# Kernel optimization log

Hardware: AMD Instinct MI355X
Metric: run time of the kernel (lower is better)

The kernel has to match this reference:

```python
import jax, jax.numpy as jnp
import numpy as np

IMG_W, IMG_H = 704, 256
BN_EPS, LN_EPS = 1e-5, 1e-5


def _l2norm(x, axis):
    n = jnp.linalg.norm(x, axis=axis, keepdims=True)
    return x / jnp.maximum(n, 1e-12)


def _layernorm(x, g, b):
    m = jnp.mean(x, axis=-1, keepdims=True)
    v = jnp.var(x, axis=-1, keepdims=True)
    return (x - m) / jnp.sqrt(v + LN_EPS) * g + b


def _bilinear(ref, uv):
    # ref: (B, d, H, W); uv: (B, P, 2) pixel coords (x, y)
    B, d, H, W = ref.shape
    x, y = uv[..., 0], uv[..., 1]
    x0 = jnp.floor(x); y0 = jnp.floor(y)
    wx = x - x0; wy = y - y0
    valid = (x >= 0) & (x <= W - 1) & (y >= 0) & (y <= H - 1)
    x0i = jnp.clip(x0.astype(jnp.int32), 0, W - 1)
    x1i = jnp.clip(x0i + 1, 0, W - 1)
    y0i = jnp.clip(y0.astype(jnp.int32), 0, H - 1)
    y1i = jnp.clip(y0i + 1, 0, H - 1)
    ref_t = ref.reshape(B, d, H * W).transpose(0, 2, 1)  # (B, HW, d)
    g = lambda yy, xx: jnp.take_along_axis(ref_t, (yy * W + xx)[..., None], axis=1)
    val = (g(y0i, x0i) * ((1 - wx) * (1 - wy))[..., None]
           + g(y0i, x1i) * (wx * (1 - wy))[..., None]
           + g(y1i, x0i) * ((1 - wx) * wy)[..., None]
           + g(y1i, x1i) * (wx * wy)[..., None])  # (B, P, d)
    return val, valid.astype(ref.dtype)


def setup_inputs() -> dict:
    key = jax.random.key(0)
    ks = jax.random.split(key, 12)
    b, n, fd, dim, h, w = 2, 6, 128, 128, 64, 176
    feature = jax.random.normal(ks[0], (b, n, fd, h, w), jnp.float32)
    # intrinsics ~ [[500,0,352],[0,500,128],[0,0,1]]
    K = jnp.array([[500.0, 0.0, IMG_W / 2], [0.0, 500.0, IMG_H / 2], [0.0, 0.0, 1.0]], jnp.float32)
    I_src = jnp.broadcast_to(K, (b, n, 3, 3)).copy()
    I_tar_inv = jnp.broadcast_to(jnp.linalg.inv(K), (b, 3, 3)).copy()
    # extrinsics near identity: small rotation + small translation
    a = 0.02 * jax.random.normal(ks[1], (b, n, 3), jnp.float32)
    zeros = jnp.zeros((b, n), jnp.float32)
    skew = jnp.stack([
        jnp.stack([zeros, -a[..., 2], a[..., 1]], -1),
        jnp.stack([a[..., 2], zeros, -a[..., 0]], -1),
        jnp.stack([-a[..., 1], a[..., 0], zeros], -1)], -2)
    R = jnp.eye(3, dtype=jnp.float32) + skew
    T = 0.1 * jax.random.normal(ks[2], (b, n, 3, 1), jnp.float32)
    E = jnp.broadcast_to(jnp.eye(4, dtype=jnp.float32), (b, n, 4, 4)).copy()
    E = E.at[..., :3, :3].set(R).at[..., :3, 3:4].set(T)
    dis = 1.5 * jnp.ones((b, 1, 1, 1), jnp.float32)
    norm = jnp.array([0.0, 0.0, 1.0], jnp.float32)[None, None] + 0.01 * jax.random.normal(ks[3], (b, 1, 3), jnp.float32)
    s = 1.0 / np.sqrt(fd)
    return {
        'feature': feature, 'I_src': I_src, 'I_tar_inv': I_tar_inv, 'E': E, 'dis': dis, 'norm': norm,
        'conv_w': s * jax.random.normal(ks[4], (dim, fd), jnp.float32),
        'bn_gamma': jnp.ones((fd,), jnp.float32), 'bn_beta': jnp.zeros((fd,), jnp.float32),
        'bn_mean': 0.1 * jax.random.normal(ks[5], (fd,), jnp.float32),
        'bn_var': jax.random.uniform(ks[6], (fd,), jnp.float32, 0.5, 1.5),
        'ln1_g': jnp.ones((dim,), jnp.float32), 'ln1_b': jnp.zeros((dim,), jnp.float32),
        'ln2_g': jnp.ones((dim,), jnp.float32), 'ln2_b': jnp.zeros((dim,), jnp.float32),
        'mlp_w1': s * jax.random.normal(ks[7], (dim, 2 * dim), jnp.float32),
        'mlp_b1': jnp.zeros((2 * dim,), jnp.float32),
        'mlp_w2': (1.0 / np.sqrt(2 * fd)) * jax.random.normal(ks[8], (2 * dim, dim), jnp.float32),
        'mlp_b2': jnp.zeros((dim,), jnp.float32),
    }


def reference(feature, I_src, I_tar_inv, E, dis, norm, conv_w, bn_gamma, bn_beta, bn_mean, bn_var,
              ln1_g, ln1_b, ln2_g, ln2_b, mlp_w1, mlp_b1, mlp_w2, mlp_b2):
    b, n, fd, h, w = feature.shape
    dim = conv_w.shape[0]
    P = h * w
    # ---- pixel grid in [0,1], homogeneous ----
    xs = jnp.linspace(0.0, 1.0, w, dtype=feature.dtype)
    ys = jnp.linspace(0.0, 1.0, h, dtype=feature.dtype)
    X, Y = jnp.meshgrid(xs, ys)  # (h, w), x varies along width
    pix = jnp.stack([X, Y, jnp.ones_like(X)], 0).reshape(3, P)  # (3, P)
    img_wh1 = jnp.array([[IMG_W], [IMG_H], [1.0]], feature.dtype)  # (3,1)
    pix = pix * img_wh1
    # ---- homography H = I_src (R - T n^T / dis) I_tar_inv ----
    R = E[..., :3, :3]
    T = E[..., :3, 3:4]
    Hm = I_src @ (R - (T @ norm[:, None, :, :]) / dis) @ I_tar_inv[:, None, :, :]  # (b,n,3,3)
    homo = jnp.einsum('bnij,jp->bnip', Hm, pix)  # (b,n,3,P)
    homo = homo[:, :, :2] / homo[:, :, 2:]
    homo = homo / img_wh1[:2]  # back to 0..1
    uv = homo.transpose(0, 1, 3, 2).reshape(b * n, P, 2) * jnp.array([w, h], feature.dtype)
    # ---- feature_linear: BN(eval) -> ReLU -> 1x1 conv ----
    xf = (feature - bn_mean[:, None, None]) / jnp.sqrt(bn_var + BN_EPS)[:, None, None]
    xf = xf * bn_gamma[:, None, None] + bn_beta[:, None, None]
    xf = jax.nn.relu(xf)
    val = jnp.einsum('oc,bnchw->bnohw', conv_w, xf)  # (b,n,dim,h,w)
    query = val[:, 0]  # (b,dim,h,w)
    # ---- homography-guided bilinear sampling ----
    v, mask = _bilinear(val.reshape(b * n, dim, h, w), uv)  # (bn,P,dim), (bn,P)
    key_n = _l2norm(v, axis=2).reshape(b, n, P, dim)
    q = _l2norm(query.reshape(b, dim, P), axis=1)
    dot = jnp.einsum('bdp,bnpd->bnp', q, key_n)
    dot = dot * mask.reshape(b, n, P)
    att = jax.nn.softmax(dot, axis=1)
    z = jnp.einsum('bnp,bnpd->bpd', att, v.reshape(b, n, P, dim))
    z = z.transpose(0, 2, 1).reshape(b, dim, h, w)
    z = query + z
    # ---- MLP block ----
    z = z.reshape(b, dim, P).transpose(0, 2, 1)  # (b,P,dim)
    z = _layernorm(z, ln1_g, ln1_b)
    hdn = jax.nn.gelu(z @ mlp_w1 + mlp_b1, approximate=False)
    z = z + (hdn @ mlp_w2 + mlp_b2)
    z = _layernorm(z, ln2_g, ln2_b)
    return z.transpose(0, 2, 1).reshape(b, dim, h, w)
```

## Files before the change

### kernel.cpp

```cpp
#include <hip/hip_runtime.h>
#include <hip/hip_bf16.h>
#include <cstdint>
#include <cstddef>

#define B_   2
#define N_   6
#define FD_  128
#define DIM_ 128
#define H_   64
#define W_   176
#define P_   (H_*W_)
#define IMGW 704.0
#define IMGH 256.0
#define UVB  8

struct __align__(16) Samp { float wx, wy; int o00, o01; int o10, o11; int valid, pad; };

typedef __attribute__((ext_vector_type(8))) short short8;
typedef __attribute__((ext_vector_type(4))) float f32x4;

__device__ __forceinline__ float wave_sum(float v) {
#pragma unroll
  for (int off = 32; off > 0; off >>= 1) v += __shfl_xor(v, off, 64);
  return v;
}

__device__ __forceinline__ unsigned short f2bf(float f) {
  union { __hip_bfloat16 h; unsigned short u; } c;
  c.h = __float2bfloat16(f);
  return c.u;
}
__device__ __forceinline__ float bf2f(unsigned short s) {
  return __uint_as_float(((unsigned int)s) << 16);
}

__global__ __launch_bounds__(256) void prep_kernel(const float* __restrict__ I_src, const float* __restrict__ I_tar_inv,
                           const float* __restrict__ E, const float* __restrict__ dis,
                           const float* __restrict__ nrm,
                           const float* __restrict__ bn_g, const float* __restrict__ bn_b,
                           const float* __restrict__ bn_m, const float* __restrict__ bn_v,
                           const float* __restrict__ w1, const float* __restrict__ w2,
                           const float* __restrict__ conv_w,
                           Samp* __restrict__ samp, float* __restrict__ bns, float* __restrict__ bnb,
                           short* __restrict__ w1b, short* __restrict__ w2b, short* __restrict__ cwb) {
  int blk = blockIdx.x;
  if (blk >= B_ * N_ * UVB) {
    int tid = (blk - B_ * N_ * UVB) * 256 + threadIdx.x;
    int f = tid >> 6, l = tid & 63;
    if (f < 64) {
      int nt = f >> 2, ks = f & 3;
      int n = nt * 16 + (l & 15);
      int kb = ks * 32 + (l >> 4) * 8;
#pragma unroll
      for (int j = 0; j < 8; ++j)
        w1b[((size_t)f * 64 + l) * 8 + j] = (short)f2bf(w1[(size_t)(kb + j) * 256 + n]);
    } else if (f < 128) {
      int g = f - 64;
      int nt = g >> 3, ks = g & 7;
      int n = nt * 16 + (l & 15);
      int kb = ks * 32 + (l >> 4) * 8;
#pragma unroll
      for (int j = 0; j < 8; ++j)
        w2b[((size_t)g * 64 + l) * 8 + j] = (short)f2bf(w2[(size_t)(kb + j) * 128 + n]);
    } else {
      int g2 = f - 128;
      int ot = g2 >> 2, ks = g2 & 3;
      int o  = ot * 16 + (l & 15);
      int cb = ks * 32 + (l >> 4) * 8;
#pragma unroll
      for (int j = 0; j < 8; ++j)
        cwb[((size_t)g2 * 64 + l) * 8 + j] = (short)f2bf(conv_w[(size_t)o * FD_ + cb + j]);
    }
    return;
  }
  int bn = blk / UVB;
  int part = blk % UVB;
  int bb = bn / N_;
  if (blk == 0 && threadIdx.x < FD_) {
    int t = threadIdx.x;
    float inv = 1.0f / sqrtf(bn_v[t] + 1e-5f);
    float sc = bn_g[t] * inv;
    bns[t] = sc;
    bnb[t] = bn_b[t] - bn_m[t] * sc;
  }
  const float* Ep = E + bn * 16;
  double R[9], T[3];
#pragma unroll
  for (int i = 0; i < 3; ++i) {
#pragma unroll
    for (int j = 0; j < 3; ++j) R[i*3+j] = (double)Ep[i*4+j];
    T[i] = (double)Ep[i*4+3];
  }
  double dd = (double)dis[bb];
  double M[9];
#pragma unroll
  for (int i = 0; i < 3; ++i)
#pragma unroll
    for (int j = 0; j < 3; ++j)
      M[i*3+j] = R[i*3+j] - T[i] * (double)nrm[bb*3+j] / dd;
  const float* Is = I_src + bn * 9;
  double A[9];
#pragma unroll
  for (int i = 0; i < 3; ++i)
#pragma unroll
    for (int j = 0; j < 3; ++j)
      A[i*3+j] = (double)Is[i*3+0]*M[0+j] + (double)Is[i*3+1]*M[3+j] + (double)Is[i*3+2]*M[6+j];
  const float* It = I_tar_inv + bb * 9;
  double Hm[9];
#pragma unroll
  for (int i = 0; i < 3; ++i)
#pragma unroll
    for (int j = 0; j < 3; ++j)
      Hm[i*3+j] = A[i*3+0]*(double)It[0+j] + A[i*3+1]*(double)It[3+j] + A[i*3+2]*(double)It[6+j];

  const double dx = 1.0 / (double)(W_ - 1);
  const double dy = 1.0 / (double)(H_ - 1);
  for (int p = part * 256 + threadIdx.x; p < P_; p += 256 * UVB) {
    int ii = p / W_;
    int jj = p - ii * W_;
    double xs = (jj == W_ - 1) ? 1.0 : (double)jj * dx;
    double ys = (ii == H_ - 1) ? 1.0 : (double)ii * dy;
    double px = xs * IMGW;
    double py = ys * IMGH;
    double hx = Hm[0]*px + Hm[1]*py + Hm[2];
    double hy = Hm[3]*px + Hm[4]*py + Hm[5];
    double hz = Hm[6]*px + Hm[7]*py + Hm[8];
    double u = ((hx / hz) / IMGW) * (double)W_;
    double v = ((hy / hz) / IMGH) * (double)H_;
    double x0 = floor(u), y0 = floor(v);
    bool valid = (u >= 0.0) && (u <= (double)(W_ - 1)) && (v >= 0.0) && (v <= (double)(H_ - 1));
    int x0i = min(max((int)x0, 0), W_ - 1);
    int x1i = min(x0i + 1, W_ - 1);
    int y0i = min(max((int)y0, 0), H_ - 1);
    int y1i = min(y0i + 1, H_ - 1);
    Samp s;
    s.wx = (float)(u - x0);
    s.wy = (float)(v - y0);
    s.o00 = (y0i * W_ + x0i) * DIM_;
    s.o01 = (y0i * W_ + x1i) * DIM_;
    s.o10 = (y1i * W_ + x0i) * DIM_;
    s.o11 = (y1i * W_ + x1i) * DIM_;
    s.valid = valid ? 1 : 0;
    s.pad = 0;
    samp[(size_t)bn * P_ + p] = s;
  }
}

__global__ __launch_bounds__(256) void conv_kernel(const float* __restrict__ feature,
    const short* __restrict__ cwb, const float* __restrict__ bns_g, const float* __restrict__ bnb_g,
    unsigned short* __restrict__ val_t) {
  __shared__ __align__(16) short xhi[128 * 66];
  __shared__ __align__(16) short xlo[128 * 66];
  __shared__ float bns_s[FD_], bnb_s[FD_];
  int t = threadIdx.x;

  if (t < FD_) { bns_s[t] = bns_g[t]; bnb_s[t] = bnb_g[t]; }
  __syncthreads();

  int bn = blockIdx.y;
  int p0 = blockIdx.x * 64;
  const float* fb = feature + (size_t)bn * FD_ * P_ + p0;

#pragma unroll
  for (int k = 0; k < 8; ++k) {
    int f4 = t + 256 * k;
    int c  = f4 >> 4;
    int pq = (f4 & 15) * 4;
    float4 x = *(const float4*)(fb + (size_t)c * P_ + pq);
    float s = bns_s[c], o = bnb_s[c];
    float v0 = fmaxf(x.x * s + o, 0.f);
    float v1 = fmaxf(x.y * s + o, 0.f);
    float v2 = fmaxf(x.z * s + o, 0.f);
    float v3 = fmaxf(x.w * s + o, 0.f);
    unsigned short h0 = f2bf(v0), h1 = f2bf(v1), h2 = f2bf(v2), h3 = f2bf(v3);
    unsigned short l0 = f2bf(v0 - bf2f(h0)), l1 = f2bf(v1 - bf2f(h1));
    unsigned short l2 = f2bf(v2 - bf2f(h2)), l3 = f2bf(v3 - bf2f(h3));
    short* dh = &xhi[c * 66 + pq];
    short* dl = &xlo[c * 66 + pq];
    dh[0] = (short)h0; dh[1] = (short)h1; dh[2] = (short)h2; dh[3] = (short)h3;
    dl[0] = (short)l0; dl[1] = (short)l1; dl[2] = (short)l2; dl[3] = (short)l3;
  }
  __syncthreads();

  int lane = t & 63, wv = t >> 6;
  int m = lane & 15, quad = lane >> 4;
  int pw = wv * 16;

  short8 Ah[4], Al[4];
#pragma unroll
  for (int ks = 0; ks < 4; ++ks) {
#pragma unroll
    for (int j = 0; j < 8; ++j) {
      int c = ks * 32 + quad * 8 + j;
      Ah[ks][j] = xhi[c * 66 + pw + m];
      Al[ks][j] = xlo[c * 66 + pw + m];
    }
  }

  f32x4 acc[8];
#pragma unroll
  for (int ot = 0; ot < 8; ++ot) {
    f32x4 a = {0.f, 0.f, 0.f, 0.f};
#pragma unroll
    for (int ks = 0; ks < 4; ++ks) {
      short8 Bv = *(const short8*)(cwb + ((size_t)(ot * 4 + ks) * 64 + lane) * 8);
      a = __builtin_amdgcn_mfma_f32_16x16x32_bf16(Ah[ks], Bv, a, 0, 0, 0);
      a = __builtin_amdgcn_mfma_f32_16x16x32_bf16(Al[ks], Bv, a, 0, 0, 0);
    }
    acc[ot] = a;
  }

  unsigned short* vb = val_t + ((size_t)bn * P_ + p0 + pw + quad * 4) * DIM_ + m;
#pragma unroll
  for (int ot = 0; ot < 8; ++ot)
#pragma unroll
    for (int r = 0; r < 4; ++r)
      vb[(size_t)r * DIM_ + ot * 16] = f2bf(acc[ot][r]);
}

__global__ __launch_bounds__(256) void attn_kernel(const unsigned short* __restrict__ val_t,
    const Samp* __restrict__ samp,
    const float* __restrict__ ln1g, const float* __restrict__ ln1b,
    float* __restrict__ zln) {
  int lane = threadIdx.x & 63;
  int wv = threadIdx.x >> 6;
  int bid = blockIdx.x;
  int newbid = (bid & 7) * (gridDim.x >> 3) + (bid >> 3);
  int pt = newbid * 4 + wv;
  if (pt >= B_ * P_) return;
  int bb = pt / P_;
  int p = pt - bb * P_;
  int d0 = lane << 1;

  unsigned int uq = *(const unsigned int*)(val_t + ((size_t)(bb * N_) * P_ + p) * DIM_ + d0);
  float qx = bf2f((unsigned short)(uq & 0xffffu));
  float qy = bf2f((unsigned short)(uq >> 16));
  float qss = wave_sum(qx * qx + qy * qy);
  float qinv = 1.0f / fmaxf(sqrtf(qss), 1e-12f);

  float dots[N_], vs0[N_], vs1[N_];
#pragma unroll
  for (int n = 0; n < N_; ++n) {
    Samp s = samp[(size_t)(bb * N_ + n) * P_ + p];
    const unsigned short* base = val_t + (size_t)(bb * N_ + n) * P_ * DIM_ + d0;
    unsigned int u00 = *(const unsigned int*)(base + s.o00);
    unsigned int u01 = *(const unsigned int*)(base + s.o01);
    unsigned int u10 = *(const unsigned int*)(base + s.o10);
    unsigned int u11 = *(const unsigned int*)(base + s.o11);
    float wx = s.wx, wy = s.wy;
    float w00 = (1.0f - wx) * (1.0f - wy), w01 = wx * (1.0f - wy);
    float w10 = (1.0f - wx) * wy,          w11 = wx * wy;
    float v0 = bf2f((unsigned short)(u00 & 0xffffu)) * w00 + bf2f((unsigned short)(u01 & 0xffffu)) * w01
             + bf2f((unsigned short)(u10 & 0xffffu)) * w10 + bf2f((unsigned short)(u11 & 0xffffu)) * w11;
    float v1 = bf2f((unsigned short)(u00 >> 16)) * w00 + bf2f((unsigned short)(u01 >> 16)) * w01
             + bf2f((unsigned short)(u10 >> 16)) * w10 + bf2f((unsigned short)(u11 >> 16)) * w11;
    float ss = v0 * v0 + v1 * v1;
    float du = qx * v0 + qy * v1;
#pragma unroll
    for (int off = 32; off > 0; off >>= 1) {
      ss += __shfl_xor(ss, off, 64);
      du += __shfl_xor(du, off, 64);
    }
    float kinv = 1.0f / fmaxf(sqrtf(ss), 1e-12f);
    dots[n] = s.valid ? (du * kinv * qinv) : 0.0f;
    vs0[n] = v0; vs1[n] = v1;
  }
  float mx = dots[0];
#pragma unroll
  for (int n = 1; n < N_; ++n) mx = fmaxf(mx, dots[n]);
  float es[N_], den = 0.f;
#pragma unroll
  for (int n = 0; n < N_; ++n) { es[n] = expf(dots[n] - mx); den += es[n]; }
  float dinv = 1.0f / den;
  float z0 = qx, z1 = qy;
#pragma unroll
  for (int n = 0; n < N_; ++n) { float a = es[n] * dinv; z0 += a * vs0[n]; z1 += a * vs1[n]; }
  float mean = wave_sum(z0 + z1) * (1.0f / DIM_);
  float c0 = z0 - mean, c1 = z1 - mean;
  float var = wave_sum(c0 * c0 + c1 * c1) * (1.0f / DIM_);
  float rstd = rsqrtf(var + 1e-5f);
  float o0 = c0 * rstd * ln1g[d0]     + ln1b[d0];
  float o1 = c1 * rstd * ln1g[d0 + 1] + ln1b[d0 + 1];
  *(float2*)(zln + (size_t)pt * DIM_ + d0) = make_float2(o0, o1);
}

__global__ __launch_bounds__(512) void mlp_kernel(const float* __restrict__ zln,
    const short* __restrict__ w1b, const short* __restrict__ w2b,
    const float* __restrict__ b1, const float* __restrict__ b2,
    const float* __restrict__ ln2g, const float* __restrict__ ln2b,
    float* __restrict__ out) {
  __shared__ __align__(16) char smem[34816];
  int t = threadIdx.x;
  int row0 = blockIdx.x * 64;

  float* zl = (float*)smem;
#pragma unroll
  for (int k = 0; k < 4; ++k) {
    int idx = t + 512 * k;
    int r = idx >> 5, c4 = (idx & 31) * 4;
    *(float4*)&zl[r * 132 + c4] = *(const float4*)(zln + (size_t)(row0 + r) * DIM_ + c4);
  }
  __syncthreads();

  int lane = t & 63, wv = t >> 6, m = lane & 15, quad = lane >> 4;
  int pt = wv & 3, ng = wv >> 2;
  int pw = pt * 16;

  short8 A1h[4], A1l[4];
#pragma unroll
  for (int ks = 0; ks < 4; ++ks) {
    const float* zr = &zl[(pw + m) * 132 + ks * 32 + quad * 8];
#pragma unroll
    for (int j = 0; j < 8; ++j) {
      float v = zr[j];
      unsigned short h = f2bf(v);
      A1h[ks][j] = (short)h;
      A1l[ks][j] = (short)f2bf(v - bf2f(h));
    }
  }
  float res[4][4];
#pragma unroll
  for (int i = 0; i < 4; ++i)
#pragma unroll
    for (int r = 0; r < 4; ++r)
      res[i][r] = zl[(pw + quad * 4 + r) * 132 + (ng * 4 + i) * 16 + m];

  float b1v[2][4];
#pragma unroll
  for (int h = 0; h < 2; ++h)
#pragma unroll
    for (int i = 0; i < 4; ++i) b1v[h][i] = b1[(h * 8 + ng * 4 + i) * 16 + m];
  float b2v[4], g2v[4], be2v[4];
#pragma unroll
  for (int i = 0; i < 4; ++i) {
    int d = (ng * 4 + i) * 16 + m;
    b2v[i] = b2[d]; g2v[i] = ln2g[d]; be2v[i] = ln2b[d];
  }
  __syncthreads();

  short* hh = (short*)smem;
  short* hl = (short*)(smem + 17408);

  f32x4 acc2[4];
#pragma unroll
  for (int i = 0; i < 4; ++i) acc2[i] = (f32x4){0.f, 0.f, 0.f, 0.f};

#pragma unroll
  for (int h = 0; h < 2; ++h) {
    if (h) __syncthreads();
#pragma unroll
    for (int i = 0; i < 4; ++i) {
      int nt = h * 8 + ng * 4 + i;
      f32x4 a = {0.f, 0.f, 0.f, 0.f};
#pragma unroll
      for (int ks = 0; ks < 4; ++ks) {
        short8 Bv = *(const short8*)(w1b + ((size_t)(nt * 4 + ks) * 64 + lane) * 8);
        a = __builtin_amdgcn_mfma_f32_16x16x32_bf16(A1h[ks], Bv, a, 0, 0, 0);
        a = __builtin_amdgcn_mfma_f32_16x16x32_bf16(A1l[ks], Bv, a, 0, 0, 0);
      }
#pragma unroll
      for (int r = 0; r < 4; ++r) {
        float hv = a[r] + b1v[h][i];
        float g = 0.5f * hv * (1.0f + erff(hv * 0.70710678118654752f));
        unsigned short gh = f2bf(g);
        int addr = (pw + quad * 4 + r) * 136 + (ng * 4 + i) * 16 + m;
        hh[addr] = (short)gh;
        hl[addr] = (short)f2bf(g - bf2f(gh));
      }
    }
    __syncthreads();
#pragma unroll
    for (int ks2 = 0; ks2 < 4; ++ks2) {
      short8 A2h = *(const short8*)&hh[(pw + m) * 136 + ks2 * 32 + quad * 8];
      short8 A2l = *(const short8*)&hl[(pw + m) * 136 + ks2 * 32 + quad * 8];
#pragma unroll
      for (int i = 0; i < 4; ++i) {
        int g = (ng * 4 + i) * 8 + h * 4 + ks2;
        short8 Bv = *(const short8*)(w2b + ((size_t)g * 64 + lane) * 8);
        acc2[i] = __builtin_amdgcn_mfma_f32_16x16x32_bf16(A2h, Bv, acc2[i], 0, 0, 0);
        acc2[i] = __builtin_amdgcn_mfma_f32_16x16x32_bf16(A2l, Bv, acc2[i], 0, 0, 0);
      }
    }
  }

  float z2[4][4];
#pragma unroll
  for (int i = 0; i < 4; ++i)
#pragma unroll
    for (int r = 0; r < 4; ++r)
      z2[i][r] = acc2[i][r] + b2v[i] + res[i][r];

  __syncthreads();
  float* pbuf = (float*)smem;
  float ps[4];
#pragma unroll
  for (int r = 0; r < 4; ++r) {
    float s = z2[0][r] + z2[1][r] + z2[2][r] + z2[3][r];
    s += __shfl_xor(s, 1, 64); s += __shfl_xor(s, 2, 64);
    s += __shfl_xor(s, 4, 64); s += __shfl_xor(s, 8, 64);
    ps[r] = s;
  }
  if (m == 0) {
#pragma unroll
    for (int r = 0; r < 4; ++r) pbuf[ng * 64 + pw + quad * 4 + r] = ps[r];
  }
  __syncthreads();
  float mean[4];
#pragma unroll
  for (int r = 0; r < 4; ++r) {
    int px = pw + quad * 4 + r;
    mean[r] = (pbuf[px] + pbuf[64 + px]) * (1.0f / 128.0f);
  }
  float pv[4];
#pragma unroll
  for (int r = 0; r < 4; ++r) {
    float vv = 0.f;
#pragma unroll
    for (int i = 0; i < 4; ++i) { float d = z2[i][r] - mean[r]; vv += d * d; }
    vv += __shfl_xor(vv, 1, 64); vv += __shfl_xor(vv, 2, 64);
    vv += __shfl_xor(vv, 4, 64); vv += __shfl_xor(vv, 8, 64);
    pv[r] = vv;
  }
  if (m == 0) {
#pragma unroll
    for (int r = 0; r < 4; ++r) pbuf[128 + ng * 64 + pw + quad * 4 + r] = pv[r];
  }
  __syncthreads();
  float rstd[4];
#pragma unroll
  for (int r = 0; r < 4; ++r) {
    int px = pw + quad * 4 + r;
    rstd[r] = rsqrtf((pbuf[128 + px] + pbuf[192 + px]) * (1.0f / 128.0f) + 1e-5f);
  }

  __syncthreads();
  float* zo = (float*)smem;
#pragma unroll
  for (int i = 0; i < 4; ++i)
#pragma unroll
    for (int r = 0; r < 4; ++r) {
      float v = (z2[i][r] - mean[r]) * rstd[r] * g2v[i] + be2v[i];
      zo[((ng * 4 + i) * 16 + m) * 68 + pw + quad * 4 + r] = v;
    }
  __syncthreads();

  int bb2 = row0 / P_;
  int p0 = row0 - bb2 * P_;
#pragma unroll
  for (int it = 0; it < 4; ++it) {
    int d = it * 32 + (t >> 4);
    int pq = (t & 15) * 4;
    float4 v4 = *(float4*)&zo[d * 68 + pq];
    *(float4*)(out + (size_t)bb2 * DIM_ * P_ + (size_t)d * P_ + p0 + pq) = v4;
  }
}

extern "C" void kernel_launch(void* const* d_in, const int* in_sizes, int n_in,
                              void* d_out, int out_size, void* d_ws, size_t ws_size,
                              hipStream_t stream) {
  const float* feature = (const float*)d_in[0];
  const float* I_src   = (const float*)d_in[1];
  const float* I_tar   = (const float*)d_in[2];
  const float* E       = (const float*)d_in[3];
  const float* dis     = (const float*)d_in[4];
  const float* nrm     = (const float*)d_in[5];
  const float* conv_w  = (const float*)d_in[6];
  const float* bn_g    = (const float*)d_in[7];
  const float* bn_b    = (const float*)d_in[8];
  const float* bn_m    = (const float*)d_in[9];
  const float* bn_v    = (const float*)d_in[10];
  const float* ln1g    = (const float*)d_in[11];
  const float* ln1b    = (const float*)d_in[12];
  const float* ln2g    = (const float*)d_in[13];
  const float* ln2b    = (const float*)d_in[14];
  const float* w1      = (const float*)d_in[15];
  const float* b1      = (const float*)d_in[16];
  const float* w2      = (const float*)d_in[17];
  const float* b2      = (const float*)d_in[18];
  float* out = (float*)d_out;

  float* wsf = (float*)d_ws;
  float* bns = wsf;
  float* bnb = wsf + 128;
  unsigned short* val_t = (unsigned short*)(wsf + 256);
  float* zln = (float*)(val_t + (size_t)B_ * N_ * P_ * DIM_);
  Samp*  samp = (Samp*)(zln + (size_t)B_ * P_ * DIM_);
  short* w1b = (short*)(samp + (size_t)B_ * N_ * P_);
  short* w2b = w1b + 32768;
  short* cwb = w2b + 32768;

  hipLaunchKernelGGL(prep_kernel, dim3(B_ * N_ * UVB + 40), dim3(256), 0, stream,
                     I_src, I_tar, E, dis, nrm, bn_g, bn_b, bn_m, bn_v, w1, w2, conv_w,
                     samp, bns, bnb, w1b, w2b, cwb);
  hipLaunchKernelGGL(conv_kernel, dim3(P_ / 64, B_ * N_), dim3(256), 0, stream,
                     feature, cwb, bns, bnb, val_t);
  hipLaunchKernelGGL(attn_kernel, dim3(B_ * P_ / 4), dim3(256), 0, stream,
                     val_t, samp, ln1g, ln1b, zln);
  hipLaunchKernelGGL(mlp_kernel, dim3(B_ * P_ / 64), dim3(512), 0, stream,
                     zln, w1b, w2b, b1, b2, ln2g, ln2b, out);
}
```

Before: 208.9 us.

## Halve MLP block size, double-buffer hidden tiles, fuse LayerNorm stat reductions

The MLP kernel now handles 32 rows per 256-thread block instead of 64 rows per 512 threads, which doubles the grid. The two GELU hidden halves are written to separate shared-memory buffers, so both first-GEMM halves run before the second GEMM and several barriers go away. The second LayerNorm computes sum and sum of squares in one reduction pass (variance as E[x^2]-mean^2), removing one barrier round. This trades some numerical robustness in the variance, and more blocks re-reading the weights, for fewer synchronisations and better occupancy.

```diff
diff --git a/kernel.cpp b/kernel.cpp
--- a/kernel.cpp
+++ b/kernel.cpp
@@ -284,26 +284,26 @@
   *(float2*)(zln + (size_t)pt * DIM_ + d0) = make_float2(o0, o1);
 }
 
-__global__ __launch_bounds__(512) void mlp_kernel(const float* __restrict__ zln,
+__global__ __launch_bounds__(256) void mlp_kernel(const float* __restrict__ zln,
     const short* __restrict__ w1b, const short* __restrict__ w2b,
     const float* __restrict__ b1, const float* __restrict__ b2,
     const float* __restrict__ ln2g, const float* __restrict__ ln2b,
     float* __restrict__ out) {
   __shared__ __align__(16) char smem[34816];
   int t = threadIdx.x;
-  int row0 = blockIdx.x * 64;
+  int row0 = blockIdx.x * 32;
 
   float* zl = (float*)smem;
 #pragma unroll
   for (int k = 0; k < 4; ++k) {
-    int idx = t + 512 * k;
+    int idx = t + 256 * k;
     int r = idx >> 5, c4 = (idx & 31) * 4;
     *(float4*)&zl[r * 132 + c4] = *(const float4*)(zln + (size_t)(row0 + r) * DIM_ + c4);
   }
   __syncthreads();
 
   int lane = t & 63, wv = t >> 6, m = lane & 15, quad = lane >> 4;
-  int pt = wv & 3, ng = wv >> 2;
+  int pt = wv & 1, ng = wv >> 1;
   int pw = pt * 16;
 
   short8 A1h[4], A1l[4];
@@ -336,50 +336,83 @@
     int d = (ng * 4 + i) * 16 + m;
     b2v[i] = b2[d]; g2v[i] = ln2g[d]; be2v[i] = ln2b[d];
   }
-  __syncthreads();
-
-  short* hh = (short*)smem;
-  short* hl = (short*)(smem + 17408);
+
+  short* hh0 = (short*)(smem + 17408);
+  short* hl0 = (short*)(smem + 26112);
+  short* hh1 = (short*)smem;
+  short* hl1 = (short*)(smem + 8704);
 
   f32x4 acc2[4];
 #pragma unroll
   for (int i = 0; i < 4; ++i) acc2[i] = (f32x4){0.f, 0.f, 0.f, 0.f};
 
 #pragma unroll
-  for (int h = 0; h < 2; ++h) {
-    if (h) __syncthreads();
+  for (int i = 0; i < 4; ++i) {
+    int nt = 0 * 8 + ng * 4 + i;
+    f32x4 a = {0.f, 0.f, 0.f, 0.f};
+#pragma unroll
+    for (int ks = 0; ks < 4; ++ks) {
+      short8 Bv = *(const short8*)(w1b + ((size_t)(nt * 4 + ks) * 64 + lane) * 8);
+      a = __builtin_amdgcn_mfma_f32_16x16x32_bf16(A1h[ks], Bv, a, 0, 0, 0);
+      a = __builtin_amdgcn_mfma_f32_16x16x32_bf16(A1l[ks], Bv, a, 0, 0, 0);
+    }
+#pragma unroll
+    for (int r = 0; r < 4; ++r) {
+      float hv = a[r] + b1v[0][i];
+      float g = 0.5f * hv * (1.0f + erff(hv * 0.70710678118654752f));
+      unsigned short gh = f2bf(g);
+      int addr = (pw + quad * 4 + r) * 136 + (ng * 4 + i) * 16 + m;
+      hh0[addr] = (short)gh;
+      hl0[addr] = (short)f2bf(g - bf2f(gh));
+    }
+  }
+  __syncthreads();
+
+#pragma unroll
+  for (int i = 0; i < 4; ++i) {
+    int nt = 1 * 8 + ng * 4 + i;
+    f32x4 a = {0.f, 0.f, 0.f, 0.f};
+#pragma unroll
+    for (int ks = 0; ks < 4; ++ks) {
+      short8 Bv = *(const short8*)(w1b + ((size_t)(nt * 4 + ks) * 64 + lane) * 8);
+      a = __builtin_amdgcn_mfma_f32_16x16x32_bf16(A1h[ks], Bv, a, 0, 0, 0);
+      a = __builtin_amdgcn_mfma_f32_16x16x32_bf16(A1l[ks], Bv, a, 0, 0, 0);
+    }
+#pragma unroll
+    for (int r = 0; r < 4; ++r) {
+      float hv = a[r] + b1v[1][i];
+      float g = 0.5f * hv * (1.0f + erff(hv * 0.70710678118654752f));
+      unsigned short gh = f2bf(g);
+      int addr = (pw + quad * 4 + r) * 136 + (ng * 4 + i) * 16 + m;
+      hh1[addr] = (short)gh;
+      hl1[addr] = (short)f2bf(g - bf2f(gh));
+    }
+  }
+
+#pragma unroll
+  for (int ks2 = 0; ks2 < 4; ++ks2) {
+    short8 A2h = *(const short8*)&hh0[(pw + m) * 136 + ks2 * 32 + quad * 8];
+    short8 A2l = *(const short8*)&hl0[(pw + m) * 136 + ks2 * 32 + quad * 8];
 #pragma unroll
     for (int i = 0; i < 4; ++i) {
-      int nt = h * 8 + ng * 4 + i;
-      f32x4 a = {0.f, 0.f, 0.f, 0.f};
-#pragma unroll
-      for (int ks = 0; ks < 4; ++ks) {
-        short8 Bv = *(const short8*)(w1b + ((size_t)(nt * 4 + ks) * 64 + lane) * 8);
-        a = __builtin_amdgcn_mfma_f32_16x16x32_bf16(A1h[ks], Bv, a, 0, 0, 0);
-        a = __builtin_amdgcn_mfma_f32_16x16x32_bf16(A1l[ks], Bv, a, 0, 0, 0);
-      }
-#pragma unroll
-      for (int r = 0; r < 4; ++r) {
-        float hv = a[r] + b1v[h][i];
-        float g = 0.5f * hv * (1.0f + erff(hv * 0.70710678118654752f));
-        unsigned short gh = f2bf(g);
-        int addr = (pw + quad * 4 + r) * 136 + (ng * 4 + i) * 16 + m;
-        hh[addr] = (short)gh;
-        hl[addr] = (short)f2bf(g - bf2f(gh));
-      }
-    }
-    __syncthreads();
-#pragma unroll
-    for (int ks2 = 0; ks2 < 4; ++ks2) {
-      short8 A2h = *(const short8*)&hh[(pw + m) * 136 + ks2 * 32 + quad * 8];
-      short8 A2l = *(const short8*)&hl[(pw + m) * 136 + ks2 * 32 + quad * 8];
-#pragma unroll
-      for (int i = 0; i < 4; ++i) {
-        int g = (ng * 4 + i) * 8 + h * 4 + ks2;
-        short8 Bv = *(const short8*)(w2b + ((size_t)g * 64 + lane) * 8);
-        acc2[i] = __builtin_amdgcn_mfma_f32_16x16x32_bf16(A2h, Bv, acc2[i], 0, 0, 0);
-        acc2[i] = __builtin_amdgcn_mfma_f32_16x16x32_bf16(A2l, Bv, acc2[i], 0, 0, 0);
-      }
+      int g = (ng * 4 + i) * 8 + 0 * 4 + ks2;
+      short8 Bv = *(const short8*)(w2b + ((size_t)g * 64 + lane) * 8);
+      acc2[i] = __builtin_amdgcn_mfma_f32_16x16x32_bf16(A2h, Bv, acc2[i], 0, 0, 0);
+      acc2[i] = __builtin_amdgcn_mfma_f32_16x16x32_bf16(A2l, Bv, acc2[i], 0, 0, 0);
+    }
+  }
+  __syncthreads();
+
+#pragma unroll
+  for (int ks2 = 0; ks2 < 4; ++ks2) {
+    short8 A2h = *(const short8*)&hh1[(pw + m) * 136 + ks2 * 32 + quad * 8];
+    short8 A2l = *(const short8*)&hl1[(pw + m) * 136 + ks2 * 32 + quad * 8];
+#pragma unroll
+    for (int i = 0; i < 4; ++i) {
+      int g = (ng * 4 + i) * 8 + 1 * 4 + ks2;
+      short8 Bv = *(const short8*)(w2b + ((size_t)g * 64 + lane) * 8);
+      acc2[i] = __builtin_amdgcn_mfma_f32_16x16x32_bf16(A2h, Bv, acc2[i], 0, 0, 0);
+      acc2[i] = __builtin_amdgcn_mfma_f32_16x16x32_bf16(A2l, Bv, acc2[i], 0, 0, 0);
     }
   }
 
@@ -390,57 +423,45 @@
     for (int r = 0; r < 4; ++r)
       z2[i][r] = acc2[i][r] + b2v[i] + res[i][r];
 
-  __syncthreads();
-  float* pbuf = (float*)smem;
-  float ps[4];
+  float* pbuf = (float*)(smem + 17408);
+  float ps[4], pq2[4];
 #pragma unroll
   for (int r = 0; r < 4; ++r) {
     float s = z2[0][r] + z2[1][r] + z2[2][r] + z2[3][r];
-    s += __shfl_xor(s, 1, 64); s += __shfl_xor(s, 2, 64);
-    s += __shfl_xor(s, 4, 64); s += __shfl_xor(s, 8, 64);
-    ps[r] = s;
+    float q2 = z2[0][r]*z2[0][r] + z2[1][r]*z2[1][r] + z2[2][r]*z2[2][r] + z2[3][r]*z2[3][r];
+#pragma unroll
+    for (int off = 1; off <= 8; off <<= 1) {
+      s  += __shfl_xor(s,  off, 64);
+      q2 += __shfl_xor(q2, off, 64);
+    }
+    ps[r] = s; pq2[r] = q2;
   }
   if (m == 0) {
 #pragma unroll
-    for (int r = 0; r < 4; ++r) pbuf[ng * 64 + pw + quad * 4 + r] = ps[r];
-  }
-  __syncthreads();
-  float mean[4];
+    for (int r = 0; r < 4; ++r) {
+      pbuf[ng * 32 + pw + quad * 4 + r]      = ps[r];
+      pbuf[64 + ng * 32 + pw + quad * 4 + r] = pq2[r];
+    }
+  }
+  __syncthreads();
+  float mean[4], rstd[4];
 #pragma unroll
   for (int r = 0; r < 4; ++r) {
     int px = pw + quad * 4 + r;
-    mean[r] = (pbuf[px] + pbuf[64 + px]) * (1.0f / 128.0f);
-  }
-  float pv[4];
-#pragma unroll
-  for (int r = 0; r < 4; ++r) {
-    float vv = 0.f;
-#pragma unroll
-    for (int i = 0; i < 4; ++i) { float d = z2[i][r] - mean[r]; vv += d * d; }
-    vv += __shfl_xor(vv, 1, 64); vv += __shfl_xor(vv, 2, 64);
-    vv += __shfl_xor(vv, 4, 64); vv += __shfl_xor(vv, 8, 64);
-    pv[r] = vv;
-  }
-  if (m == 0) {
-#pragma unroll
-    for (int r = 0; r < 4; ++r) pbuf[128 + ng * 64 + pw + quad * 4 + r] = pv[r];
-  }
-  __syncthreads();
-  float rstd[4];
-#pragma unroll
-  for (int r = 0; r < 4; ++r) {
-    int px = pw + quad * 4 + r;
-    rstd[r] = rsqrtf((pbuf[128 + px] + pbuf[192 + px]) * (1.0f / 128.0f) + 1e-5f);
-  }
-
-  __syncthreads();
+    mean[r] = (pbuf[px] + pbuf[32 + px]) * (1.0f / 128.0f);
+    float msq = (pbuf[64 + px] + pbuf[96 + px]) * (1.0f / 128.0f);
+    float var = fmaxf(msq - mean[r] * mean[r], 0.f);
+    rstd[r] = rsqrtf(var + 1e-5f);
+  }
+  __syncthreads();
+
   float* zo = (float*)smem;
 #pragma unroll
   for (int i = 0; i < 4; ++i)
 #pragma unroll
     for (int r = 0; r < 4; ++r) {
       float v = (z2[i][r] - mean[r]) * rstd[r] * g2v[i] + be2v[i];
-      zo[((ng * 4 + i) * 16 + m) * 68 + pw + quad * 4 + r] = v;
+      zo[((ng * 4 + i) * 16 + m) * 36 + pw + quad * 4 + r] = v;
     }
   __syncthreads();
 
@@ -448,9 +469,9 @@
   int p0 = row0 - bb2 * P_;
 #pragma unroll
   for (int it = 0; it < 4; ++it) {
-    int d = it * 32 + (t >> 4);
-    int pq = (t & 15) * 4;
-    float4 v4 = *(float4*)&zo[d * 68 + pq];
+    int d = it * 32 + (t >> 3);
+    int pq = (t & 7) * 4;
+    float4 v4 = *(float4*)&zo[d * 36 + pq];
     *(float4*)(out + (size_t)bb2 * DIM_ * P_ + (size_t)d * P_ + p0 + pq) = v4;
   }
 }
@@ -496,6 +517,6 @@
                      feature, cwb, bns, bnb, val_t);
   hipLaunchKernelGGL(attn_kernel, dim3(B_ * P_ / 4), dim3(256), 0, stream,
                      val_t, samp, ln1g, ln1b, zln);
-  hipLaunchKernelGGL(mlp_kernel, dim3(B_ * P_ / 64), dim3(512), 0, stream,
+  hipLaunchKernelGGL(mlp_kernel, dim3(B_ * P_ / 32), dim3(256), 0, stream,
                      zln, w1b, w2b, b1, b2, ln2g, ln2b, out);
 }
```

Result: faster. 198.9 us (-4.8%).
